# Optimization experiments

Hardware: AMD Instinct MI355X
Metric: run time of the kernel (lower is better)

The kernel has to match this reference:

```python
import jax, jax.numpy as jnp
import numpy as np
import math

B, C, H, W, M = 8, 256, 128, 128, 7
EPS = 1e-08


def setup_inputs() -> dict:
    key = jax.random.key(0)
    ks = jax.random.split(key, 7)
    x_high = jax.random.normal(ks[0], (B, C, H // 2, W // 2), jnp.float32)
    x_low = jax.random.normal(ks[1], (B, C, H, W), jnp.float32)
    w1 = jax.random.normal(ks[2], (32, M * M), jnp.float32) / np.sqrt(M * M)
    b1 = jnp.zeros((32,), jnp.float32)
    w2 = jax.random.normal(ks[3], (3, 32), jnp.float32) / np.sqrt(32)
    b2 = jnp.zeros((3,), jnp.float32)
    refine_w = jax.random.normal(ks[4], (C, C), jnp.float32) / np.sqrt(C)
    return {"x_high": x_high, "x_low": x_low, "w1": w1, "b1": b1,
            "w2": w2, "b2": b2, "refine_w": refine_w}


def _anisotropic_kernel(params):
    # params: (B,3) -> normalized Gaussian kernels (B, m, m)
    theta = jnp.arctan2(params[:, 0], params[:, 1]) / 2.0 + math.pi / 2.0
    lam1 = jnp.exp(params[:, 2])
    lam2 = 1.0 / (lam1 + EPS)
    coords = jnp.arange(M, dtype=jnp.float32) - (M // 2)  # -3..3
    yy = coords[:, None]  # (m,1) varies along rows (torch meshgrid 'ij')
    xx = coords[None, :]  # (1,m)
    cos_t = jnp.cos(theta)[:, None, None]
    sin_t = jnp.sin(theta)[:, None, None]
    x_rot = xx * cos_t + yy * sin_t          # (B,m,m)
    y_rot = -xx * sin_t + yy * cos_t
    l1 = lam1[:, None, None]
    l2 = lam2[:, None, None]
    k = jnp.exp(-(x_rot ** 2 / (2.0 * l1 ** 2) + y_rot ** 2 / (2.0 * l2 ** 2)))
    return k / (jnp.sum(k, axis=(1, 2), keepdims=True) + EPS)


def _depthwise(x, kern):
    # x: (B,C,H,W), kern: (B,m,m) -> per-sample depthwise conv, kernel shared across C
    k = jnp.repeat(kern, C, axis=0)[:, None, :, :]  # (B*C,1,m,m)
    pad = M // 2
    y = jax.lax.conv_general_dilated(
        x.reshape(1, B * C, H, W), k, (1, 1), [(pad, pad), (pad, pad)],
        dimension_numbers=("NCHW", "OIHW", "NCHW"), feature_group_count=B * C)
    return y.reshape(B, C, H, W)


def reference(x_high, x_low, w1, b1, w2, b2, refine_w):
    # bilinear upsample (align_corners=False == half-pixel, matches jax.image.resize)
    x_high_up = jax.image.resize(x_high, (B, C, H, W), method="bilinear")

    x_f = jnp.fft.fftshift(jnp.fft.fft2(x_low, norm="ortho"), axes=(-2, -1))
    real, imag = jnp.real(x_f), jnp.imag(x_f)
    mag = jnp.abs(x_f)
    mag_weighted = jnp.mean(mag, axis=1, keepdims=True)  # (B,1,H,W)
    h0, w0 = H // 2 - M // 2, W // 2 - M // 2
    mag_center = mag_weighted[:, :, h0:h0 + M, w0:w0 + M]  # (B,1,m,m)

    # param_net: Flatten -> Linear -> ReLU -> Linear
    flat = mag_center.reshape(B, M * M)
    h = jax.nn.relu(flat @ w1.T + b1)
    params = h @ w2.T + b2  # (B,3)

    kern = _anisotropic_kernel(params)
    real_f = _depthwise(real, kern)
    imag_f = _depthwise(imag, kern)

    # 1x1 refine conv (bias-free), shared for real and imag parts
    real_f = jnp.einsum("bchw,oc->bohw", real_f, refine_w)
    imag_f = jnp.einsum("bchw,oc->bohw", imag_f, refine_w)

    out_f = jax.lax.complex(real_f, imag_f)
    out_f = jnp.fft.ifftshift(out_f, axes=(-2, -1))
    x_low_enhanced = jnp.real(jnp.fft.ifft2(out_f, norm="ortho"))
    return x_low_enhanced + x_high_up
```

## Files before the change

kernel.cpp:

```cpp
#include <hip/hip_runtime.h>

typedef __attribute__((ext_vector_type(8))) short bf16x8;
typedef __attribute__((ext_vector_type(4))) float f32x4;
typedef __attribute__((ext_vector_type(4))) int   i32x4;

#define PI_F 3.14159265358979323846f
#define C128 0.0490873852123405f
#define INV_SQRT128 0.0883883476483184f
#define INV128 0.0078125f

#define NB 8
#define NC 256
#define NH 128
#define NW 128
#define IMG 16384
#define NIMG 2048

#define GH_STRIDE 3200
#define AB_STRIDE 3072

__device__ __forceinline__ unsigned short f2bf(float f){
  unsigned int u = __float_as_uint(f);
  u += 0x7FFFu + ((u >> 16) & 1u);
  return (unsigned short)(u >> 16);
}
__device__ __forceinline__ float bf2f(unsigned short u){
  return __uint_as_float(((unsigned int)u) << 16);
}

__device__ __constant__ int c_pcnt[6] = {1,2,3,3,2,1};
__device__ __constant__ int c_pdp0[6] = {6,5,4,0,0,0};

#define COS1 0.9987954562051724f
#define SIN1 0.0490676743274180f
#define K1CH (2.0f*COS1)

#define SM_GG   8320
#define SM_HLR  9344
#define SM_HLI  9856
#define SM_SCRG 1920

__global__ void __launch_bounds__(512, 8) K1(const float* __restrict__ xlow,
                                             float* __restrict__ GH){
  __shared__ float smem[10240];
  unsigned short* xs = (unsigned short*)smem;
  const int tid = threadIdx.x;
  const int img = blockIdx.x;
  float* ghb = GH + (size_t)img*GH_STRIDE;

  {
    const float4* xp = (const float4*)(xlow + (size_t)img*IMG);
    #pragma unroll
    for (int k=0; k<8; ++k){
      int e4 = k*512 + tid;
      float4 v = xp[e4];
      int r = e4 >> 5, c = (e4 & 31)*4;
      unsigned int pw0 = (unsigned int)f2bf(v.x) | ((unsigned int)f2bf(v.y) << 16);
      unsigned int pw1 = (unsigned int)f2bf(v.z) | ((unsigned int)f2bf(v.w) << 16);
      *(unsigned int*)(&xs[r*130 + c    ]) = pw0;
      *(unsigned int*)(&xs[r*130 + c + 2]) = pw1;
    }
  }
  __syncthreads();

  float acc[14];
  #pragma unroll
  for (int i=0;i<14;++i) acc[i]=0.f;

  const int isRow = (tid < 256);
  const int lid  = isRow ? tid : (tid-256);
  const int idx  = lid & 127;
  const int half = lid >> 7;

  {
    const float sg0 = half ? -1.f : 1.f;
    float cp = sg0, sp = 0.f;
    float cn = sg0*COS1, sn = sg0*SIN1;

#define K1_ACCUM(xv, cc, ss)                                   \
    {                                                          \
      float t2 = cc + cc;                                      \
      float c2 = fmaf(t2, cc, -1.f);                           \
      float s2 = t2 * ss;                                      \
      float c3 = fmaf(t2, c2, -cc);                            \
      float s3 = fmaf(t2, s2, -ss);                            \
      acc[0 + PARITY] += xv;                                   \
      acc[2 + PARITY*2]  = fmaf(xv, cc, acc[2 + PARITY*2]);    \
      acc[3 + PARITY*2]  = fmaf(xv, ss, acc[3 + PARITY*2]);    \
      acc[6 + PARITY*2]  = fmaf(xv, c2, acc[6 + PARITY*2]);    \
      acc[7 + PARITY*2]  = fmaf(xv, s2, acc[7 + PARITY*2]);    \
      acc[10 + PARITY*2] = fmaf(xv, c3, acc[10 + PARITY*2]);   \
      acc[11 + PARITY*2] = fmaf(xv, s3, acc[11 + PARITY*2]);   \
    }

    if (isRow){
      const unsigned short* xr = &xs[idx*130 + half*64];
      #pragma unroll 4
      for (int j=0; j<32; ++j){
        unsigned int pk = *(const unsigned int*)(&xr[2*j]);
        float xe = __uint_as_float(pk << 16);
        float xo = __uint_as_float(pk & 0xffff0000u);
#define PARITY 0
        K1_ACCUM(xe, cp, sp)
#undef PARITY
#define PARITY 1
        K1_ACCUM(xo, cn, sn)
#undef PARITY
        float cpn = fmaf(K1CH, cn, -cp);
        float spn = fmaf(K1CH, sn, -sp);
        float cnn = fmaf(K1CH, cpn, -cn);
        float snn = fmaf(K1CH, spn, -sn);
        cp = cpn; sp = spn; cn = cnn; sn = snn;
      }
    } else {
      const unsigned short* xc = &xs[half*64*130 + idx];
      #pragma unroll 4
      for (int j=0; j<32; ++j){
        float xe = bf2f(xc[(2*j  )*130]);
        float xo = bf2f(xc[(2*j+1)*130]);
#define PARITY 0
        K1_ACCUM(xe, cp, sp)
#undef PARITY
#define PARITY 1
        K1_ACCUM(xo, cn, sn)
#undef PARITY
        float cpn = fmaf(K1CH, cn, -cp);
        float spn = fmaf(K1CH, sn, -sp);
        float cnn = fmaf(K1CH, cpn, -cn);
        float snn = fmaf(K1CH, spn, -sn);
        cp = cpn; sp = spn; cn = cnn; sn = snn;
      }
    }
#undef K1_ACCUM
  }
  __syncthreads();

  const int scrbase = (isRow ? 0 : SM_SCRG) + idx*15;
  if (half){
    #pragma unroll
    for (int i=0;i<14;++i) smem[scrbase+i] = acc[i];
  }
  __syncthreads();
  if (!half){
    #pragma unroll
    for (int i=0;i<14;++i) acc[i] += smem[scrbase+i];
    float A0e=acc[0],A0o=acc[1],Ce1=acc[2],Se1=acc[3],Co1=acc[4],So1=acc[5],
          Ce2=acc[6],Se2=acc[7],Co2=acc[8],So2=acc[9],
          Ce3=acc[10],Se3=acc[11],Co3=acc[12],So3=acc[13];
    float d0  = A0e-A0o;
    float dc1 = Ce1-Co1, ds1 = Se1-So1;
    float dc2 = Ce2-Co2, ds2 = Se2-So2;
    float dc3 = Ce3-Co3, ds3 = Se3-So3;
    float* gp = ghb + (isRow ? 1536 : 0);
    const int k = idx;
    gp[(0*2+0)*128+k] = dc3*INV_SQRT128;  gp[(0*2+1)*128+k] =  ds3*INV_SQRT128;
    gp[(1*2+0)*128+k] = dc2*INV_SQRT128;  gp[(1*2+1)*128+k] =  ds2*INV_SQRT128;
    gp[(2*2+0)*128+k] = dc1*INV_SQRT128;  gp[(2*2+1)*128+k] =  ds1*INV_SQRT128;
    gp[(3*2+0)*128+k] = d0 *INV_SQRT128;  gp[(3*2+1)*128+k] =  0.f;
    gp[(4*2+0)*128+k] = dc1*INV_SQRT128;  gp[(4*2+1)*128+k] = -ds1*INV_SQRT128;
    gp[(5*2+0)*128+k] = dc2*INV_SQRT128;  gp[(5*2+1)*128+k] = -ds2*INV_SQRT128;
    if (isRow){
      smem[SM_HLR + 0*128 + k] = A0e+A0o;
      smem[SM_HLR + 1*128 + k] = Ce1+Co1;
      smem[SM_HLR + 2*128 + k] = Ce2+Co2;
      smem[SM_HLR + 3*128 + k] = Ce3+Co3;
      smem[SM_HLI + 0*128 + k] = -(Se1+So1);
      smem[SM_HLI + 1*128 + k] = -(Se2+So2);
      smem[SM_HLI + 2*128 + k] = -(Se3+So3);
    } else {
      smem[SM_GG + (0*2+0)*128 + k] = dc3;  smem[SM_GG + (0*2+1)*128 + k] = ds3;
      smem[SM_GG + (1*2+0)*128 + k] = dc2;  smem[SM_GG + (1*2+1)*128 + k] = ds2;
      smem[SM_GG + (2*2+0)*128 + k] = dc1;  smem[SM_GG + (2*2+1)*128 + k] = ds1;
      smem[SM_GG + (3*2+0)*128 + k] = d0;   smem[SM_GG + (3*2+1)*128 + k] = 0.f;
    }
  }
  __syncthreads();

  if (tid < 144){
    int out = tid >> 2, chunk = tid & 3;
    int wi = out/6, zi = out%6, z = 61+zi;
    int wsrc = (wi<4) ? wi : (wi==4 ? 2 : 1);
    float isg = (wi<4) ? 1.f : -1.f;
    float fR=0.f, fI=0.f;
    const int cEnd = chunk*32 + 32;
    for (int c=chunk*32; c<cEnd; ++c){
      float gR = smem[SM_GG + (wsrc*2  )*128 + c];
      float gI = isg*smem[SM_GG + (wsrc*2+1)*128 + c];
      int m = (z*c) & 127;
      float ts, tc; __sincosf((float)m*C128, &ts, &tc);
      fR += gR*tc + gI*ts;
      fI += gI*tc - gR*ts;
    }
    fR += __shfl_xor(fR,1); fI += __shfl_xor(fI,1);
    fR += __shfl_xor(fR,2); fI += __shfl_xor(fI,2);
    if (chunk==0){
      ghb[3072 + out*2]     = fR * INV128;
      ghb[3072 + out*2 + 1] = fI * INV128;
    }
  }
  if (tid >= 256 && tid < 452){
    int i = (tid-256) >> 2, chunk = (tid-256) & 3;
    int u = i/7 - 3, v = i%7 - 3;
    int va = v < 0 ? -v : v;
    float vsg = v < 0 ? -1.f : 1.f;
    float fR=0.f, fI=0.f;
    const int rEnd = chunk*32 + 32;
    for (int r=chunk*32; r<rEnd; ++r){
      float hR = smem[SM_HLR + va*128 + r];
      float hI = (va==0) ? 0.f : vsg*smem[SM_HLI + (va-1)*128 + r];
      int m = ((u*r) % 128 + 128) & 127;
      float ts, tc; __sincosf((float)m*C128, &ts, &tc);
      fR += hR*tc + hI*ts;
      fI += hI*tc - hR*ts;
    }
    fR += __shfl_xor(fR,1); fI += __shfl_xor(fI,1);
    fR += __shfl_xor(fR,2); fI += __shfl_xor(fI,2);
    if (chunk==0){
      fR *= INV128; fI *= INV128;
      ghb[3144 + i] = sqrtf(fR*fR + fI*fI);
    }
  }
}

__global__ void __launch_bounds__(64) K_mlp(const float* __restrict__ GH,
                                            const float* __restrict__ w1,
                                            const float* __restrict__ b1,
                                            const float* __restrict__ w2,
                                            const float* __restrict__ b2,
                                            float* __restrict__ kern){
  __shared__ float flat[49];
  __shared__ float hh[32];
  const int b = blockIdx.x, tid = threadIdx.x;
  if (tid < 49){
    float s = 0.f;
    for (int c=0; c<256; ++c)
      s += GH[(size_t)(b*256 + c)*GH_STRIDE + 3144 + tid];
    flat[tid] = s * (1.0f/256.0f);
  }
  __syncthreads();
  if (tid < 32){
    float s = b1[tid];
    for (int i=0; i<49; ++i) s += flat[i]*w1[tid*49+i];
    hh[tid] = fmaxf(s, 0.f);
  }
  __syncthreads();
  if (tid == 0){
    float p[3];
    #pragma unroll
    for (int k=0; k<3; ++k){
      float s = b2[k];
      for (int j=0; j<32; ++j) s += hh[j]*w2[k*32+j];
      p[k] = s;
    }
    float theta = atan2f(p[0], p[1])*0.5f + 1.57079632679489662f;
    float ct = cosf(theta), st = sinf(theta);
    float l1 = expf(p[2]);
    float l2 = 1.0f/(l1 + 1e-8f);
    float inv1 = 1.0f/(2.0f*l1*l1);
    float inv2 = 1.0f/(2.0f*l2*l2);
    float sum = 0.f;
    for (int i=0; i<7; ++i) for (int j=0; j<7; ++j){
      float yy = (float)(i-3), xx = (float)(j-3);
      float xr =  xx*ct + yy*st;
      float yr = -xx*st + yy*ct;
      sum += expf(-(xr*xr*inv1 + yr*yr*inv2));
    }
    float inv = 1.0f/(sum + 1e-8f);
    for (int i=0; i<7; ++i) for (int j=0; j<7; ++j){
      float yy = (float)(i-3), xx = (float)(j-3);
      float xr =  xx*ct + yy*st;
      float yr = -xx*st + yy*ct;
      kern[b*49 + i*7 + j] = expf(-(xr*xr*inv1 + yr*yr*inv2)) * inv;
    }
  }
}

__global__ void __launch_bounds__(256) K3(const float* __restrict__ kern,
                                          float* __restrict__ KL,
                                          float* __restrict__ W){
  __shared__ float twc[128], tws[128], kl[49];
  __shared__ float kapl[7][2][128];
  const int b = blockIdx.x, tid = threadIdx.x;
  if (tid < 128){
    float s,c; __sincosf((float)tid*C128, &s, &c);
    twc[tid]=c; tws[tid]=s;
  }
  if (tid < 49) kl[tid] = kern[b*49 + tid];
  __syncthreads();
  if (tid < 128){
    const int c = tid;
    float* klb = KL + (size_t)b*3584;
    #pragma unroll
    for (int dp=0; dp<7; ++dp){
      float kR=0.f, kI=0.f;
      #pragma unroll
      for (int dq=0; dq<7; ++dq){
        int m = (((dq-3)*c) % 128 + 128) & 127;
        float kv = kl[dp*7+dq];
        kR += kv*twc[m]; kI -= kv*tws[m];
      }
      klb[(dp*2  )*128 + c] = kR;
      klb[(dp*2+1)*128 + c] = kI;
      kapl[dp][0][c] = kR; kapl[dp][1][c] = kI;
    }
    const int r = tid;
    #pragma unroll
    for (int dq=0; dq<7; ++dq){
      float lR=0.f, lI=0.f;
      #pragma unroll
      for (int dp=0; dp<7; ++dp){
        int m = (((dp-3)*r) % 128 + 128) & 127;
        float kv = kl[dp*7+dq];
        lR += kv*twc[m]; lI -= kv*tws[m];
      }
      klb[1792 + (dq*2  )*128 + r] = lR;
      klb[1792 + (dq*2+1)*128 + r] = lI;
    }
  }
  __syncthreads();
  for (int k=0;k<64;++k){
    int px = k*256 + tid;
    int r = px >> 7, c = px & 127;
    float w = 0.f;
    #pragma unroll
    for (int dp=0; dp<7; ++dp){
      int m = (((dp-3)*r) % 128 + 128) & 127;
      w += twc[m]*kapl[dp][0][c] + tws[m]*kapl[dp][1][c];
    }
    W[(size_t)b*IMG + px] = w;
  }
}

__global__ void __launch_bounds__(128) K_tab(const float* __restrict__ GH,
                                             const float* __restrict__ KL,
                                             const float* __restrict__ kern,
                                             float* __restrict__ AB){
  __shared__ float dRe[36], dIm[36], kl[49];
  const int tid = threadIdx.x;
  const int img = blockIdx.x, b = img >> 8;
  const float* ghb = GH + (size_t)img*GH_STRIDE;
  const float* klb = KL + (size_t)b*3584;
  float* abb = AB + (size_t)img*AB_STRIDE;

  if (tid < 49) kl[tid] = kern[b*49 + tid];
  __syncthreads();
  if (tid < 36){
    int si = tid/6, ti = tid%6;
    float dR=0.f, dI=0.f;
    for (int j=0; j<c_pcnt[si]; ++j){
      int dp = c_pdp0[si] + j;
      int wi = (si-3) + dp;
      for (int l=0; l<c_pcnt[ti]; ++l){
        int dq = c_pdp0[ti] + l;
        int zi = (ti-3) + dq;
        float kv = kl[dp*7+dq];
        dR += kv * ghb[3072 + (wi*6+zi)*2];
        dI += kv * ghb[3072 + (wi*6+zi)*2 + 1];
      }
    }
    dRe[tid] = dR; dIm[tid] = dI;
  }
  __syncthreads();

  const int c = tid;
  float s1,c1; __sincosf((float)c*C128, &s1, &c1);
  float c2 = c1*c1 - s1*s1, s2 = 2.f*c1*s1;
  float c3 = c1*c2 - s1*s2, s3 = s1*c2 + c1*s2;
  float ct[6] = {c3,c2,c1,1.f,c1,c2};
  float st[6] = {-s3,-s2,-s1,0.f,s1,s2};
  float sgnc = (c & 1) ? -1.f : 1.f;

  float gr[6], gi[6], kr[7], ki[7];
  #pragma unroll
  for (int w=0;w<6;++w){ gr[w]=ghb[(w*2)*128+c]; gi[w]=ghb[(w*2+1)*128+c]; }
  #pragma unroll
  for (int dp=0;dp<7;++dp){ kr[dp]=klb[(dp*2)*128+c]; ki[dp]=klb[(dp*2+1)*128+c]; }

  #pragma unroll
  for (int si=0; si<6; ++si){
    float dR=0.f, dI=0.f;
    for (int j=0; j<c_pcnt[si]; ++j){
      int dp = c_pdp0[si] + j;
      int w = (si-3) + dp;
      dR += kr[dp]*gr[w] - ki[dp]*gi[w];
      dI += kr[dp]*gi[w] + ki[dp]*gr[w];
    }
    float corrR=0.f, corrI=0.f;
    #pragma unroll
    for (int ti=0; ti<6; ++ti){
      float DR = dRe[si*6+ti], DI = dIm[si*6+ti];
      corrR += DR*ct[ti] - DI*st[ti];
      corrI += DR*st[ti] + DI*ct[ti];
    }
    abb[(si*2  )*128 + c] = INV_SQRT128*dR - INV128*sgnc*corrR;
    abb[(si*2+1)*128 + c] = INV_SQRT128*dI - INV128*sgnc*corrI;
  }

  const int r = tid;
  float hr[6], hi_[6], lr[7], li[7];
  #pragma unroll
  for (int z=0;z<6;++z){ hr[z]=ghb[1536+(z*2)*128+r]; hi_[z]=ghb[1536+(z*2+1)*128+r]; }
  #pragma unroll
  for (int dq=0;dq<7;++dq){ lr[dq]=klb[1792+(dq*2)*128+r]; li[dq]=klb[1792+(dq*2+1)*128+r]; }
  #pragma unroll
  for (int ti=0; ti<6; ++ti){
    float bR=0.f, bI=0.f;
    for (int l=0; l<c_pcnt[ti]; ++l){
      int dq = c_pdp0[ti] + l;
      int z = (ti-3) + dq;
      bR += lr[dq]*hr[z] - li[dq]*hi_[z];
      bI += lr[dq]*hi_[z] + li[dq]*hr[z];
    }
    abb[1536 + r*12 + ti*2]     = INV_SQRT128*bR;
    abb[1536 + r*12 + ti*2 + 1] = INV_SQRT128*bI;
  }
}

__global__ void __launch_bounds__(256) K4(const float* __restrict__ xlow,
                                          const float* __restrict__ W,
                                          const float* __restrict__ AB,
                                          unsigned short* __restrict__ filt){
  const int tid = threadIdx.x;
  const int img = blockIdx.x, b = img >> 8;
  const int c0 = (tid & 63)*2, grp = tid >> 6;
  const float* abb = AB + (size_t)img*AB_STRIDE;
  const float* xim = xlow + (size_t)img*IMG;
  const float* Wb  = W + (size_t)b*IMG;
  unsigned short* fim = filt + (size_t)img*IMG;

  float ar[2][6], ai[2][6], ctc[2][6], stc[2][6];
  #pragma unroll
  for (int col=0; col<2; ++col){
    int c = c0 + col;
    #pragma unroll
    for (int si=0;si<6;++si){ ar[col][si]=abb[(si*2)*128+c]; ai[col][si]=abb[(si*2+1)*128+c]; }
    float s1,c1; __sincosf((float)c*C128, &s1, &c1);
    float c2 = c1*c1 - s1*s1, s2 = 2.f*c1*s1;
    float c3 = c1*c2 - s1*s2, s3 = s1*c2 + c1*s2;
    ctc[col][0]=c3; ctc[col][1]=c2; ctc[col][2]=c1; ctc[col][3]=1.f; ctc[col][4]=c1; ctc[col][5]=c2;
    stc[col][0]=-s3; stc[col][1]=-s2; stc[col][2]=-s1; stc[col][3]=0.f; stc[col][4]=s1; stc[col][5]=s2;
  }

  for (int k=0;k<32;++k){
    int ru = __builtin_amdgcn_readfirstlane(grp*32 + k);
    const float* brow = abb + 1536 + ru*12;
    float4 b0 = *(const float4*)(brow);
    float4 b1 = *(const float4*)(brow+4);
    float4 b2 = *(const float4*)(brow+8);
    float rs1,rc1; __sincosf((float)ru*C128, &rs1, &rc1);
    float rc2 = rc1*rc1 - rs1*rs1, rs2 = 2.f*rc1*rs1;
    float rc3 = rc1*rc2 - rs1*rs2, rs3 = rs1*rc2 + rc1*rs2;
    float rcs[6] = {rc3,rc2,rc1,1.f,rc1,rc2};
    float rss[6] = {-rs3,-rs2,-rs1,0.f,rs1,rs2};

    float ER0 = 0.f, ER1 = 0.f;
    #pragma unroll
    for (int si=0;si<6;++si){
      ER0 += rcs[si]*ar[0][si] - rss[si]*ai[0][si];
      ER1 += rcs[si]*ar[1][si] - rss[si]*ai[1][si];
    }
    float rsg = (ru & 1) ? -1.f : 1.f;
    ER0 *= rsg; ER1 *= rsg;

    float bRv[6] = {b0.x, b0.z, b1.x, b1.z, b2.x, b2.z};
    float bIv[6] = {b0.y, b0.w, b1.y, b1.w, b2.y, b2.w};
    float EC0 = 0.f, EC1 = 0.f;
    #pragma unroll
    for (int ti=0;ti<6;++ti){
      EC0 += ctc[0][ti]*bRv[ti] - stc[0][ti]*bIv[ti];
      EC1 += ctc[1][ti]*bRv[ti] - stc[1][ti]*bIv[ti];
    }
    int px = ru*128 + c0;
    float2 xv = *(const float2*)(&xim[px]);
    float2 wv = *(const float2*)(&Wb[px]);
    float v0 = xv.x*wv.x - ER0 - EC0;
    float v1 = xv.y*wv.y - ER1 + EC1;
    unsigned int pack = ((unsigned int)f2bf(v1) << 16) | (unsigned int)f2bf(v0);
    *(unsigned int*)(&fim[px]) = pack;
  }
}

__global__ void __launch_bounds__(256) K_w(const float* __restrict__ rw,
                                           unsigned short* __restrict__ rwbf){
  int i = blockIdx.x*256 + threadIdx.x;
  rwbf[i] = f2bf(rw[i]);
}

__global__ void __launch_bounds__(256) K_up(const float* __restrict__ xhigh,
                                            unsigned short* __restrict__ up){
  __shared__ float xs[64*68];
  const int tid = threadIdx.x;
  const int img = blockIdx.x;
  const float* src = xhigh + (size_t)img*4096;
  unsigned short* dst = up + (size_t)img*IMG;

  #pragma unroll
  for (int p=0; p<4; ++p){
    int t = p*256 + tid;
    float4 v = ((const float4*)src)[t];
    int r = t >> 4, k = t & 15;
    *(float4*)(&xs[r*68 + k*4]) = v;
  }
  __syncthreads();

  for (int k=0; k<32; ++k){
    int pr = k*256 + tid;
    int y = pr >> 6, x0 = (pr & 63)*2;
    float fy = 0.5f*(float)y - 0.25f;
    int iyf = (int)floorf(fy);
    float ty = fy - (float)iyf;
    int iy0 = iyf < 0 ? 0 : iyf;
    int iy1 = (iyf+1) > 63 ? 63 : (iyf+1);
    float wy1 = ty, wy0 = 1.0f - ty;
    const float* r0 = &xs[iy0*68];
    const float* r1 = &xs[iy1*68];

    float outv[2];
    #pragma unroll
    for (int e=0; e<2; ++e){
      int x = x0 + e;
      float fx = 0.5f*(float)x - 0.25f;
      int ixf = (int)floorf(fx);
      float tx = fx - (float)ixf;
      int ix0 = ixf < 0 ? 0 : ixf;
      int ix1 = (ixf+1) > 63 ? 63 : (ixf+1);
      float wx1 = tx, wx0 = 1.0f - tx;
      outv[e] = wy0*(wx0*r0[ix0] + wx1*r0[ix1])
              + wy1*(wx0*r1[ix0] + wx1*r1[ix1]);
    }
    unsigned int pack = ((unsigned int)f2bf(outv[1]) << 16) | (unsigned int)f2bf(outv[0]);
    *(unsigned int*)(&dst[y*NW + x0]) = pack;
  }
}

__global__ void __launch_bounds__(256, 4) K_gemm(const unsigned short* __restrict__ rwbf,
                                                 const unsigned short* __restrict__ filt,
                                                 const unsigned short* __restrict__ up,
                                                 float* __restrict__ out){
  __shared__ unsigned short At[2][128*40];
  __shared__ unsigned short Bt[2][128*40];
  const int tid = threadIdx.x, lane = tid & 63, wv = tid >> 6;
  const int wr = wv >> 1, wc = wv & 1;
  const int xg = blockIdx.x;
  const int g16 = xg >> 4, i16 = xg & 15;
  const int ot = i16 >> 3, pt = (g16 << 3) | (i16 & 7);
  const int b = blockIdx.z;
  const int p0 = pt*128, o0 = ot*128;

  f32x4 acc[4][4];
  #pragma unroll
  for (int m=0;m<4;++m)
    #pragma unroll
    for (int n=0;n<4;++n){ f32x4 z = {0.f,0.f,0.f,0.f}; acc[m][n] = z; }

  const int arow  = tid >> 2;
  const int akoff = (tid & 3) * 8;
  const unsigned short* aP0 = &rwbf[(size_t)(o0+arow   )*256 + akoff];
  const unsigned short* aP1 = &rwbf[(size_t)(o0+arow+64)*256 + akoff];

  const int bc2 = (tid & 15) * 2;
  const int bpo = (tid >> 4) * 8;
  const unsigned short* bP0 = &filt[((size_t)b*NC + bc2    )*IMG + p0 + bpo];
  const unsigned short* bP1 = &filt[((size_t)b*NC + bc2 + 1)*IMG + p0 + bpo];

  i32x4 pf[2][4];

#define LOAD_STEP(S, KS)                                                     \
  {                                                                          \
    pf[S][0] = *(const i32x4*)(aP0 + (KS)*32);                               \
    pf[S][1] = *(const i32x4*)(aP1 + (KS)*32);                               \
    pf[S][2] = *(const i32x4*)(bP0 + (size_t)(KS)*32*IMG);                   \
    pf[S][3] = *(const i32x4*)(bP1 + (size_t)(KS)*32*IMG);                   \
  }

#define STORE_STEP(BUF, S)                                                   \
  {                                                                          \
    *(i32x4*)(&At[BUF][ arow    *40 + akoff]) = pf[S][0];                    \
    *(i32x4*)(&At[BUF][(arow+64)*40 + akoff]) = pf[S][1];                    \
    _Pragma("unroll")                                                        \
    for (int j=0;j<4;++j){                                                   \
      unsigned int w0 = (unsigned int)pf[S][2][j];                           \
      unsigned int w1 = (unsigned int)pf[S][3][j];                           \
      unsigned int lo = (w0 & 0xffffu) | (w1 << 16);                         \
      unsigned int hi = (w0 >> 16) | (w1 & 0xffff0000u);                     \
      *(unsigned int*)(&Bt[BUF][(bpo+2*j  )*40 + bc2]) = lo;                 \
      *(unsigned int*)(&Bt[BUF][(bpo+2*j+1)*40 + bc2]) = hi;                 \
    }                                                                        \
  }

  LOAD_STEP(0, 0)
  LOAD_STEP(1, 1)
  STORE_STEP(0, 0)
  __syncthreads();

  const int g = lane >> 4, r16 = lane & 15;
  #pragma unroll
  for (int ks=0; ks<8; ++ks){
    const int cur = ks & 1, nxt = cur ^ 1;
    if (ks < 6) LOAD_STEP(cur, ks+2)
    bf16x8 af[4], bfr[4];
    #pragma unroll
    for (int m=0;m<4;++m) af[m]  = *(const bf16x8*)(&At[cur][(wr*64 + m*16 + r16)*40 + g*8]);
    #pragma unroll
    for (int n=0;n<4;++n) bfr[n] = *(const bf16x8*)(&Bt[cur][(wc*64 + n*16 + r16)*40 + g*8]);
    #pragma unroll
    for (int m=0;m<4;++m)
      #pragma unroll
      for (int n=0;n<4;++n)
        acc[m][n] = __builtin_amdgcn_mfma_f32_16x16x32_bf16(af[m], bfr[n], acc[m][n], 0, 0, 0);
    if (ks < 7){
      STORE_STEP(nxt, nxt)
      __syncthreads();
    }
  }
#undef LOAD_STEP
#undef STORE_STEP

  const int y = pt;
  #pragma unroll
  for (int m=0;m<4;++m){
    #pragma unroll
    for (int j=0;j<4;++j){
      int o = o0 + wr*64 + m*16 + g*4 + j;
      size_t base = (size_t)(b*NC + o)*IMG + (size_t)y*NW;
      #pragma unroll
      for (int n=0;n<4;++n){
        int xcol = wc*64 + n*16 + r16;
        float upv = bf2f(up[base + xcol]);
        out[base + xcol] = acc[m][n][j] + upv;
      }
    }
  }
}

extern "C" void kernel_launch(void* const* d_in, const int* in_sizes, int n_in,
                              void* d_out, int out_size, void* d_ws, size_t ws_size,
                              hipStream_t stream){
  (void)in_sizes; (void)n_in; (void)out_size; (void)ws_size;
  const float* xhigh = (const float*)d_in[0];
  const float* xlow  = (const float*)d_in[1];
  const float* w1    = (const float*)d_in[2];
  const float* b1    = (const float*)d_in[3];
  const float* w2    = (const float*)d_in[4];
  const float* b2    = (const float*)d_in[5];
  const float* rw    = (const float*)d_in[6];

  char* ws = (char*)d_ws;
  unsigned short* filt  = (unsigned short*)(ws);
  unsigned short* up    = (unsigned short*)(ws + 67108864);
  float* GH   = (float*)(ws + 134217728);
  float* AB   = (float*)(ws + 160432128);
  float* kern = (float*)(ws + 185597952);
  float* KL   = (float*)(ws + 185602048);
  float* Wf   = (float*)(ws + 185716736);
  unsigned short* rwbf = (unsigned short*)(ws + 186241024);

  K1   <<<NIMG, 512, 0, stream>>>(xlow, GH);
  K_mlp<<<NB,   64,  0, stream>>>(GH, w1, b1, w2, b2, kern);
  K3   <<<NB,   256, 0, stream>>>(kern, KL, Wf);
  K_w  <<<256,  256, 0, stream>>>(rw, rwbf);
  K_tab<<<NIMG, 128, 0, stream>>>(GH, KL, kern, AB);
  K4   <<<NIMG, 256, 0, stream>>>(xlow, Wf, AB, filt);
  K_up <<<NIMG, 256, 0, stream>>>(xhigh, up);
  K_gemm <<<dim3(256, 1, NB), 256, 0, stream>>>(rwbf, filt, up, (float*)d_out);
}
```

Baseline: 286.4 us.

## Parallelize channel-mean reduction, stagger smem loops, single-buffer GEMM LDS for occupancy

Moves the serial 256-channel mean in K_mlp into a new K_red kernel that launches one block per (coefficient, batch) and reduces with wave shuffles. This removes a long serial strided loop run by only 8 blocks. The DFT loops in K1 are rotated per thread to spread shared-memory bank accesses. The GEMM drops its LDS double buffer and raises the launch-bounds occupancy hint, at the cost of an extra barrier per k-step. It also adds one kernel launch.

```diff
diff --git a/kernel.cpp b/kernel.cpp
--- a/kernel.cpp
+++ b/kernel.cpp
@@ -182,8 +182,8 @@
     int wsrc = (wi<4) ? wi : (wi==4 ? 2 : 1);
     float isg = (wi<4) ? 1.f : -1.f;
     float fR=0.f, fI=0.f;
-    const int cEnd = chunk*32 + 32;
-    for (int c=chunk*32; c<cEnd; ++c){
+    for (int ii=0; ii<32; ++ii){
+      int c = chunk*32 + ((ii + tid) & 31);
       float gR = smem[SM_GG + (wsrc*2  )*128 + c];
       float gI = isg*smem[SM_GG + (wsrc*2+1)*128 + c];
       int m = (z*c) & 127;
@@ -204,8 +204,8 @@
     int va = v < 0 ? -v : v;
     float vsg = v < 0 ? -1.f : 1.f;
     float fR=0.f, fI=0.f;
-    const int rEnd = chunk*32 + 32;
-    for (int r=chunk*32; r<rEnd; ++r){
+    for (int ii=0; ii<32; ++ii){
+      int r = chunk*32 + ((ii + tid) & 31);
       float hR = smem[SM_HLR + va*128 + r];
       float hI = (va==0) ? 0.f : vsg*smem[SM_HLI + (va-1)*128 + r];
       int m = ((u*r) % 128 + 128) & 127;
@@ -222,7 +222,20 @@
   }
 }
 
-__global__ void __launch_bounds__(64) K_mlp(const float* __restrict__ GH,
+__global__ void __launch_bounds__(256) K_red(const float* __restrict__ GH,
+                                             float* __restrict__ flatb){
+  __shared__ float ws4[4];
+  const int i = blockIdx.x, b = blockIdx.y;
+  const int tid = threadIdx.x;
+  float v = GH[((size_t)(b*256 + tid))*GH_STRIDE + 3144 + i];
+  #pragma unroll
+  for (int off=1; off<64; off<<=1) v += __shfl_xor(v, off);
+  if ((tid & 63) == 0) ws4[tid >> 6] = v;
+  __syncthreads();
+  if (tid == 0) flatb[b*49 + i] = (ws4[0]+ws4[1]+ws4[2]+ws4[3]) * (1.0f/256.0f);
+}
+
+__global__ void __launch_bounds__(64) K_mlp(const float* __restrict__ flatb,
                                             const float* __restrict__ w1,
                                             const float* __restrict__ b1,
                                             const float* __restrict__ w2,
@@ -231,12 +244,7 @@
   __shared__ float flat[49];
   __shared__ float hh[32];
   const int b = blockIdx.x, tid = threadIdx.x;
-  if (tid < 49){
-    float s = 0.f;
-    for (int c=0; c<256; ++c)
-      s += GH[(size_t)(b*256 + c)*GH_STRIDE + 3144 + tid];
-    flat[tid] = s * (1.0f/256.0f);
-  }
+  if (tid < 49) flat[tid] = flatb[b*49 + tid];
   __syncthreads();
   if (tid < 32){
     float s = b1[tid];
@@ -533,12 +541,12 @@
   }
 }
 
-__global__ void __launch_bounds__(256, 4) K_gemm(const unsigned short* __restrict__ rwbf,
+__global__ void __launch_bounds__(256, 8) K_gemm(const unsigned short* __restrict__ rwbf,
                                                  const unsigned short* __restrict__ filt,
                                                  const unsigned short* __restrict__ up,
                                                  float* __restrict__ out){
-  __shared__ unsigned short At[2][128*40];
-  __shared__ unsigned short Bt[2][128*40];
+  __shared__ unsigned short At[128*40];
+  __shared__ unsigned short Bt[128*40];
   const int tid = threadIdx.x, lane = tid & 63, wv = tid >> 6;
   const int wr = wv >> 1, wc = wv & 1;
   const int xg = blockIdx.x;
@@ -573,43 +581,43 @@
     pf[S][3] = *(const i32x4*)(bP1 + (size_t)(KS)*32*IMG);                   \
   }
 
-#define STORE_STEP(BUF, S)                                                   \
+#define STORE_STEP(S)                                                        \
   {                                                                          \
-    *(i32x4*)(&At[BUF][ arow    *40 + akoff]) = pf[S][0];                    \
-    *(i32x4*)(&At[BUF][(arow+64)*40 + akoff]) = pf[S][1];                    \
+    *(i32x4*)(&At[ arow    *40 + akoff]) = pf[S][0];                         \
+    *(i32x4*)(&At[(arow+64)*40 + akoff]) = pf[S][1];                         \
     _Pragma("unroll")                                                        \
     for (int j=0;j<4;++j){                                                   \
       unsigned int w0 = (unsigned int)pf[S][2][j];                           \
       unsigned int w1 = (unsigned int)pf[S][3][j];                           \
       unsigned int lo = (w0 & 0xffffu) | (w1 << 16);                         \
       unsigned int hi = (w0 >> 16) | (w1 & 0xffff0000u);                     \
-      *(unsigned int*)(&Bt[BUF][(bpo+2*j  )*40 + bc2]) = lo;                 \
-      *(unsigned int*)(&Bt[BUF][(bpo+2*j+1)*40 + bc2]) = hi;                 \
+      *(unsigned int*)(&Bt[(bpo+2*j  )*40 + bc2]) = lo;                      \
+      *(unsigned int*)(&Bt[(bpo+2*j+1)*40 + bc2]) = hi;                      \
     }                                                                        \
   }
 
   LOAD_STEP(0, 0)
   LOAD_STEP(1, 1)
-  STORE_STEP(0, 0)
+  STORE_STEP(0)
   __syncthreads();
 
   const int g = lane >> 4, r16 = lane & 15;
   #pragma unroll
   for (int ks=0; ks<8; ++ks){
-    const int cur = ks & 1, nxt = cur ^ 1;
-    if (ks < 6) LOAD_STEP(cur, ks+2)
+    if (ks < 6) LOAD_STEP(ks & 1, ks+2)
     bf16x8 af[4], bfr[4];
     #pragma unroll
-    for (int m=0;m<4;++m) af[m]  = *(const bf16x8*)(&At[cur][(wr*64 + m*16 + r16)*40 + g*8]);
-    #pragma unroll
-    for (int n=0;n<4;++n) bfr[n] = *(const bf16x8*)(&Bt[cur][(wc*64 + n*16 + r16)*40 + g*8]);
+    for (int m=0;m<4;++m) af[m]  = *(const bf16x8*)(&At[(wr*64 + m*16 + r16)*40 + g*8]);
+    #pragma unroll
+    for (int n=0;n<4;++n) bfr[n] = *(const bf16x8*)(&Bt[(wc*64 + n*16 + r16)*40 + g*8]);
     #pragma unroll
     for (int m=0;m<4;++m)
       #pragma unroll
       for (int n=0;n<4;++n)
         acc[m][n] = __builtin_amdgcn_mfma_f32_16x16x32_bf16(af[m], bfr[n], acc[m][n], 0, 0, 0);
     if (ks < 7){
-      STORE_STEP(nxt, nxt)
+      __syncthreads();
+      STORE_STEP((ks+1) & 1)
       __syncthreads();
     }
   }
@@ -654,9 +662,11 @@
   float* KL   = (float*)(ws + 185602048);
   float* Wf   = (float*)(ws + 185716736);
   unsigned short* rwbf = (unsigned short*)(ws + 186241024);
+  float* flatb = (float*)(ws + 186372096);
 
   K1   <<<NIMG, 512, 0, stream>>>(xlow, GH);
-  K_mlp<<<NB,   64,  0, stream>>>(GH, w1, b1, w2, b2, kern);
+  K_red<<<dim3(49, NB), 256, 0, stream>>>(GH, flatb);
+  K_mlp<<<NB,   64,  0, stream>>>(flatb, w1, b1, w2, b2, kern);
   K3   <<<NB,   256, 0, stream>>>(kern, KL, Wf);
   K_w  <<<256,  256, 0, stream>>>(rw, rwbf);
   K_tab<<<NIMG, 128, 0, stream>>>(GH, KL, kern, AB);
```

After: 597.8 us, median of 2. +108.7%, slower.
